# Kernel optimization log

Hardware: AMD Instinct MI355X
Metric: run time of the kernel (lower is better)

Reference implementation:

```python
import jax, jax.numpy as jnp
import numpy as np

B, T, C = 4, 4096, 1024
NEG_INF = -1e38


def setup_inputs() -> dict:
    key = jax.random.key(0)
    ks = jax.random.split(key, 5)
    scale = 0.02  # realistic init scale for CxC projections
    x = jax.random.normal(ks[0], (B, T, C), dtype=jnp.float32)
    key_w = jax.random.normal(ks[1], (C, C), dtype=jnp.float32) * scale
    value_w = jax.random.normal(ks[2], (C, C), dtype=jnp.float32) * scale
    receptance_w = jax.random.normal(ks[3], (C, C), dtype=jnp.float32) * scale
    output_w = jax.random.normal(ks[4], (C, C), dtype=jnp.float32) * scale
    # deterministic param init matching the module's __init__
    time_decay = -5.0 + 8.0 * (jnp.arange(C, dtype=jnp.float32) / (C - 1)) ** 0.7
    time_first = jnp.full((C,), -3.0, dtype=jnp.float32)
    # initial WKV state as in forward() when state is None
    aa0 = jnp.zeros((B, C), dtype=jnp.float32)
    bb0 = jnp.zeros((B, C), dtype=jnp.float32)
    pp0 = jnp.full((B, C), NEG_INF, dtype=jnp.float32)
    return dict(x=x, key_w=key_w, value_w=value_w, receptance_w=receptance_w,
                output_w=output_w, time_decay=time_decay, time_first=time_first,
                aa0=aa0, bb0=bb0, pp0=pp0)


def reference(x, key_w, value_w, receptance_w, output_w,
              time_decay, time_first, aa0, bb0, pp0):
    # projections (torch Linear: y = x @ W.T)
    k = jnp.einsum('btc,dc->btd', x, key_w)        # [B,T,C]
    v = jnp.einsum('btc,dc->btd', x, value_w)      # [B,T,C]
    r = jax.nn.sigmoid(jnp.einsum('btc,dc->btd', x, receptance_w))
    w = jnp.exp(time_decay)  # [C]
    u = time_first           # [C]

    def step(carry, kv):
        aa, bb, pp = carry           # each [B,C]
        kt, vt = kv                  # each [B,C]
        # output at this step (numerically stabilized exp weighting)
        ww = u + kt
        p = jnp.maximum(pp, ww)
        e1 = jnp.exp(pp - p)
        e2 = jnp.exp(ww - p)
        wkv = (e1 * aa + e2 * vt) / (e1 * bb + e2)
        # state update
        ww2 = pp - w
        p2 = jnp.maximum(ww2, kt)
        e1b = jnp.exp(ww2 - p2)
        e2b = jnp.exp(kt - p2)
        return (e1b * aa + e2b * vt, e1b * bb + e2b, p2), wkv

    k_t = jnp.swapaxes(k, 0, 1)  # [T,B,C]
    v_t = jnp.swapaxes(v, 0, 1)
    (aa, bb, pp), wkv = jax.lax.scan(step, (aa0, bb0, pp0), (k_t, v_t))
    wkv = jnp.swapaxes(wkv, 0, 1)  # [B,T,C]

    out = jnp.einsum('btc,dc->btd', r * wkv, output_w)
    return out, aa, bb, pp
```

## Files before the change

### kernel.cpp

```cpp
#include <hip/hip_runtime.h>
#include <stdint.h>

#define BDIM 4
#define TDIM 4096
#define CDIM 1024
#define MDIM (BDIM * TDIM)
#define SSEG 64
#define LSEG 64
#define NCH  (BDIM * CDIM)

#define GK   1024
#define GK2  2048
#define NTK  16

typedef __attribute__((ext_vector_type(8))) short bf16x8;
typedef __attribute__((ext_vector_type(4))) float f32x4;

__device__ __forceinline__ unsigned short f2bf(float f) {
    unsigned u = __builtin_bit_cast(unsigned, f);
    u = u + 0x7fffu + ((u >> 16) & 1u);
    return (unsigned short)(u >> 16);
}
__device__ __forceinline__ float bf2f(unsigned short h) {
    unsigned u = ((unsigned)h) << 16;
    return __builtin_bit_cast(float, u);
}

typedef __attribute__((address_space(1))) const unsigned int g_u32;
typedef __attribute__((address_space(3))) unsigned int l_u32;
__device__ __forceinline__ void gload_lds16(const void* g, void* l) {
    __builtin_amdgcn_global_load_lds((g_u32*)g, (l_u32*)l, 16, 0, 0);
}

__global__ void castall(const float* __restrict__ x,
                        const float* __restrict__ kw, const float* __restrict__ vw,
                        const float* __restrict__ rw, const float* __restrict__ ow,
                        unsigned short* __restrict__ xb,
                        unsigned short* __restrict__ wf, unsigned short* __restrict__ owb) {
    int i = blockIdx.x * 256 + threadIdx.x;
    const float* s;
    unsigned short* d;
    int j;
    if (i < 4194304) {
        s = x; d = xb; j = i;
    } else {
        int k = i - 4194304;
        int m = k >> 18; j = k & 262143;
        s = (m == 0) ? kw : (m == 1) ? vw : (m == 2) ? rw : ow;
        d = (m < 3) ? (wf + (size_t)m * 1048576) : owb;
    }
    float4 f = ((const float4*)s)[j];
    ushort4 o;
    o.x = f2bf(f.x); o.y = f2bf(f.y); o.z = f2bf(f.z); o.w = f2bf(f.w);
    ((ushort4*)d)[j] = o;
}

template <int MODE, int NT>
__global__ __launch_bounds__(512, 2) void gemm256(
    const unsigned short* __restrict__ A,
    const unsigned short* __restrict__ Bw,
    unsigned short* __restrict__ oK, unsigned short* __restrict__ oV,
    unsigned short* __restrict__ oR, float* __restrict__ oF)
{
    extern __shared__ char sh[];
    char* shA = sh;
    char* shB = sh + 65536;

    const int tid  = threadIdx.x;
    const int wave = tid >> 6;
    const int lane = tid & 63;
    const int wm   = wave >> 2;
    const int wn   = wave & 3;
    const int lrow = lane & 15;
    const int koct = lane >> 4;

    const int kb0 = (koct * 16) ^ ((lrow & 7) << 4);
    const int kb1 = kb0 ^ 64;

    const int sr0  = tid >> 3;
    const int sc0  = ((tid & 7) * 16) ^ ((sr0 & 7) << 4);
    const int sr1  = (512 + tid) >> 3;
    const int sc1  = ((tid & 7) * 16) ^ ((sr1 & 7) << 4);
    const int sd0  = tid * 16;
    const int sd1  = 8192 + tid * 16;

    const int bid = blockIdx.x;
    const int xcd = bid & 7;
    const int idx = bid >> 3;
    const int mt  = xcd * 8 + idx / NT;
    const int nt  = idx % NT;
    const size_t row0 = (size_t)mt * 256;
    const size_t col0 = (size_t)nt * 256;

    const char* gA = (const char*)A  + row0 * GK2;
    const char* gB = (const char*)Bw + col0 * GK2;

    auto stage = [&](int tt, int part) {
        if (tt >= NTK) return;
        int slot = tt & 1;
        int isA  = (part < 2) ? 1 : 0;
        int half = part & 1;
        const char* gbase = (isA ? gA : gB) + (size_t)half * 128 * GK2 + tt * 128;
        char* lbase = (isA ? shA : shB) + (slot * 2 + half) * 16384;
        gload_lds16(gbase + (size_t)sr0 * GK2 + sc0, lbase + sd0);
        gload_lds16(gbase + (size_t)sr1 * GK2 + sc1, lbase + sd1);
    };

    stage(0, 0); stage(0, 1); stage(0, 2); stage(0, 3);
    stage(1, 0); stage(1, 1);
    asm volatile("s_waitcnt vmcnt(4)" ::: "memory");
    __builtin_amdgcn_s_barrier();

    f32x4 acc[8][4] = {};
    bf16x8 af[8][2], bf_[4][2];

    {
        const char* ab0 = shA + wm * 16384 + lrow * 128;
#pragma unroll
        for (int mi = 0; mi < 4; ++mi) {
            af[mi][0] = *(const bf16x8*)(ab0 + mi * 2048 + kb0);
            af[mi][1] = *(const bf16x8*)(ab0 + mi * 2048 + kb1);
        }
    }

    for (int t = 0; t < NTK; ++t) {
        const int slot  = t & 1;
        const char* ab  = shA + (slot * 2 + wm) * 16384 + lrow * 128;
        const char* bb  = shB + (slot * 2 + (wn >> 1)) * 16384 + ((wn & 1) * 64 + lrow) * 128;
        const char* abN = shA + (((t + 1) & 1) * 2 + wm) * 16384 + lrow * 128;

#pragma unroll
        for (int ni = 0; ni < 4; ++ni) {
            bf_[ni][0] = *(const bf16x8*)(bb + ni * 2048 + kb0);
            bf_[ni][1] = *(const bf16x8*)(bb + ni * 2048 + kb1);
        }
#pragma unroll
        for (int mi = 4; mi < 8; ++mi) {
            af[mi][0] = *(const bf16x8*)(ab + mi * 2048 + kb0);
            af[mi][1] = *(const bf16x8*)(ab + mi * 2048 + kb1);
        }
        stage(t + 1, 2);
        stage(t + 1, 3);
        __builtin_amdgcn_s_barrier();
        __builtin_amdgcn_s_setprio(1);
#pragma unroll
        for (int a = 0; a < 4; ++a)
#pragma unroll
            for (int b = 0; b < 4; ++b)
#pragma unroll
                for (int ks = 0; ks < 2; ++ks)
                    acc[a][b] = __builtin_amdgcn_mfma_f32_16x16x32_bf16(af[a][ks], bf_[b][ks], acc[a][b], 0, 0, 0);
        __builtin_amdgcn_s_setprio(0);
        if (t <= 14)      asm volatile("s_waitcnt vmcnt(4)" ::: "memory");
        __builtin_amdgcn_s_barrier();

        if (t + 1 < NTK) {
#pragma unroll
            for (int mi = 0; mi < 4; ++mi) {
                af[mi][0] = *(const bf16x8*)(abN + mi * 2048 + kb0);
                af[mi][1] = *(const bf16x8*)(abN + mi * 2048 + kb1);
            }
        }
        stage(t + 2, 0);
        stage(t + 2, 1);
        __builtin_amdgcn_s_barrier();
        __builtin_amdgcn_s_setprio(1);
#pragma unroll
        for (int a = 0; a < 4; ++a)
#pragma unroll
            for (int b = 0; b < 4; ++b)
#pragma unroll
                for (int ks = 0; ks < 2; ++ks)
                    acc[4 + a][b] = __builtin_amdgcn_mfma_f32_16x16x32_bf16(af[4 + a][ks], bf_[b][ks], acc[4 + a][b], 0, 0, 0);
        __builtin_amdgcn_s_setprio(0);
        if (t <= 13)      asm volatile("s_waitcnt vmcnt(4)" ::: "memory");
        else if (t == 14) asm volatile("s_waitcnt vmcnt(0)" ::: "memory");
        __builtin_amdgcn_s_barrier();
    }

    const int crow = (lane >> 4) * 4;
    const int ccol = lane & 15;
    if (MODE == 1) {
#pragma unroll
        for (int mi = 0; mi < 8; ++mi)
#pragma unroll
            for (int ni = 0; ni < 4; ++ni) {
                size_t gr = row0 + wm * 128 + mi * 16 + crow;
                size_t gc = col0 + wn * 64 + ni * 16 + ccol;
#pragma unroll
                for (int j = 0; j < 4; ++j)
                    oF[(gr + j) * 1024 + gc] = acc[mi][ni][j];
            }
    } else {
        const int region = nt >> 2;
        unsigned short* dst = (region == 0) ? oK : ((region == 1) ? oV : oR);
        const size_t cb0 = (size_t)(nt & 3) * 256;
#pragma unroll
        for (int mi = 0; mi < 8; ++mi)
#pragma unroll
            for (int ni = 0; ni < 4; ++ni) {
                size_t gr = row0 + wm * 128 + mi * 16 + crow;
                size_t gc = cb0 + wn * 64 + ni * 16 + ccol;
#pragma unroll
                for (int j = 0; j < 4; ++j) {
                    float val = acc[mi][ni][j];
                    if (region == 2) val = 1.0f / (1.0f + __expf(-val));
                    dst[(gr + j) * 1024 + gc] = f2bf(val);
                }
            }
    }
}

__global__ __launch_bounds__(256) void wkv_phase1(
    const unsigned short* __restrict__ kf, const unsigned short* __restrict__ vf,
    const float* __restrict__ td,
    float* __restrict__ segA, float* __restrict__ segB, float* __restrict__ segP)
{
    const int tid  = blockIdx.x * 256 + threadIdx.x;
    const int lane = tid & 63;
    const int wg   = tid >> 6;
    const int cg   = wg & 63;
    const int s    = wg >> 6;
    const int q    = cg * 64 + lane;
    const int b    = q >> 10;
    const int c    = q & (CDIM - 1);

    const float w = __expf(td[c]);

    float aa = 0.0f, bb = 0.0f, pp = -1e38f;
    size_t idx = (size_t)b * TDIM * CDIM + (size_t)(s * LSEG) * CDIM + c;
#pragma unroll 4
    for (int i = 0; i < LSEG; ++i, idx += CDIM) {
        float kt = bf2f(kf[idx]);
        float vt = bf2f(vf[idx]);
        float ww2 = pp - w;
        float p2  = fmaxf(ww2, kt);
        float e1  = __expf(ww2 - p2);
        float e2  = __expf(kt - p2);
        aa = e1 * aa + e2 * vt;
        bb = e1 * bb + e2;
        pp = p2;
    }
    segA[s * NCH + q] = aa;
    segB[s * NCH + q] = bb;
    segP[s * NCH + q] = pp;
}

__global__ __launch_bounds__(256) void wkv_phase2(
    const float* __restrict__ segA, const float* __restrict__ segB, const float* __restrict__ segP,
    const float* __restrict__ td,
    const float* __restrict__ aa0, const float* __restrict__ bb0, const float* __restrict__ pp0,
    float* __restrict__ preA, float* __restrict__ preB, float* __restrict__ preP,
    float* __restrict__ stout)
{
    const int tid = blockIdx.x * 256 + threadIdx.x;
    const int c = tid & (CDIM - 1);
    const float w  = __expf(td[c]);
    const float Lw = (float)LSEG * w;

    float aa = aa0[tid], bb = bb0[tid], pp = pp0[tid];
    for (int s = 0; s < SSEG; ++s) {
        preA[s * NCH + tid] = aa;
        preB[s * NCH + tid] = bb;
        preP[s * NCH + tid] = pp;
        float al = segA[s * NCH + tid];
        float bl = segB[s * NCH + tid];
        float pl = segP[s * NCH + tid];
        float ppd = pp - Lw;
        float p  = fmaxf(ppd, pl);
        float e1 = __expf(ppd - p);
        float e2 = __expf(pl - p);
        aa = e1 * aa + e2 * al;
        bb = e1 * bb + e2 * bl;
        pp = p;
    }
    stout[tid]           = aa;
    stout[NCH + tid]     = bb;
    stout[2 * NCH + tid] = pp;
}

__global__ __launch_bounds__(256) void wkv_phase3(
    const unsigned short* __restrict__ kf, const unsigned short* __restrict__ vf,
    const unsigned short* __restrict__ rb,
    const float* __restrict__ td, const float* __restrict__ tf,
    const float* __restrict__ preA, const float* __restrict__ preB, const float* __restrict__ preP,
    unsigned short* __restrict__ rwkvb)
{
    const int tid  = blockIdx.x * 256 + threadIdx.x;
    const int lane = tid & 63;
    const int wg   = tid >> 6;
    const int cg   = wg & 63;
    const int s    = wg >> 6;
    const int q    = cg * 64 + lane;
    const int b    = q >> 10;
    const int c    = q & (CDIM - 1);

    const float w = __expf(td[c]);
    const float u = tf[c];

    float aa = preA[s * NCH + q];
    float bb = preB[s * NCH + q];
    float pp = preP[s * NCH + q];

    size_t idx = (size_t)b * TDIM * CDIM + (size_t)(s * LSEG) * CDIM + c;
#pragma unroll 4
    for (int i = 0; i < LSEG; ++i, idx += CDIM) {
        float kt = bf2f(kf[idx]);
        float vt = bf2f(vf[idx]);
        float rt = bf2f(rb[idx]);
        float ww = u + kt;
        float p  = fmaxf(pp, ww);
        float e1 = __expf(pp - p);
        float e2 = __expf(ww - p);
        float wkv = (e1 * aa + e2 * vt) / (e1 * bb + e2);
        rwkvb[idx] = f2bf(rt * wkv);
        float ww2 = pp - w;
        float p2  = fmaxf(ww2, kt);
        float e1b = __expf(ww2 - p2);
        float e2b = __expf(kt - p2);
        aa = e1b * aa + e2b * vt;
        bb = e1b * bb + e2b;
        pp = p2;
    }
}

extern "C" void kernel_launch(void* const* d_in, const int* in_sizes, int n_in,
                              void* d_out, int out_size, void* d_ws, size_t ws_size,
                              hipStream_t stream) {
    const float* x   = (const float*)d_in[0];
    const float* kw  = (const float*)d_in[1];
    const float* vw  = (const float*)d_in[2];
    const float* rw  = (const float*)d_in[3];
    const float* ow  = (const float*)d_in[4];
    const float* td  = (const float*)d_in[5];
    const float* tf  = (const float*)d_in[6];
    const float* aa0 = (const float*)d_in[7];
    const float* bb0 = (const float*)d_in[8];
    const float* pp0 = (const float*)d_in[9];
    float* out = (float*)d_out;

    char* ws = (char*)d_ws;
    unsigned short* wf    = (unsigned short*)(ws);
    unsigned short* owb   = (unsigned short*)(ws + 6291456);
    unsigned short* xb    = (unsigned short*)(ws + 8388608);
    unsigned short* kfb   = (unsigned short*)(ws + 41943040);
    unsigned short* vfb   = (unsigned short*)(ws + 75497472);
    unsigned short* rbb   = (unsigned short*)(ws + 109051904);
    unsigned short* rwkvb = (unsigned short*)(ws + 142606336);
    float* segA = (float*)(ws + 176160768);
    float* segB = (float*)(ws + 177209344);
    float* segP = (float*)(ws + 178257920);
    float* preA = (float*)(ws + 179306496);
    float* preB = (float*)(ws + 180355072);
    float* preP = (float*)(ws + 181403648);

    hipFuncSetAttribute((const void*)(gemm256<0, 12>), hipFuncAttributeMaxDynamicSharedMemorySize, 131072);
    hipFuncSetAttribute((const void*)(gemm256<1, 4>),  hipFuncAttributeMaxDynamicSharedMemorySize, 131072);

    castall<<<20480, 256, 0, stream>>>(x, kw, vw, rw, ow, xb, wf, owb);

    gemm256<0, 12><<<768, 512, 131072, stream>>>(xb, wf, kfb, vfb, rbb, nullptr);

    wkv_phase1<<<NCH * SSEG / 256, 256, 0, stream>>>(kfb, vfb, td, segA, segB, segP);
    wkv_phase2<<<NCH / 256, 256, 0, stream>>>(segA, segB, segP, td, aa0, bb0, pp0,
                                              preA, preB, preP, out + (size_t)MDIM * CDIM);
    wkv_phase3<<<NCH * SSEG / 256, 256, 0, stream>>>(kfb, vfb, rbb, td, tf,
                                                     preA, preB, preP, rwkvb);

    gemm256<1, 4><<<256, 512, 131072, stream>>>(rwkvb, owb, nullptr, nullptr, nullptr, out);
}
```

Before: 219.5 us.

## Restructure GEMM mainloop to 32-wide K tiles with four-stage LDS pipeline

The GEMM main loop now steps through K in 32-element tiles (64 bytes) instead of 64-element tiles, keeping four LDS slots in flight with three tiles prefetched. The swizzled LDS layout is reworked so each fragment is one 16-byte read, and B fragments are double-buffered in registers across iterations. The goal is deeper prefetch to hide global-load latency at the same LDS footprint. In exchange there are twice as many barriers and waitcnt points per unit of K work, and each global load row is shorter.

```diff
diff --git a/kernel.cpp b/kernel.cpp
--- a/kernel.cpp
+++ b/kernel.cpp
@@ -11,7 +11,7 @@
 
 #define GK   1024
 #define GK2  2048
-#define NTK  16
+#define NT32 32
 
 typedef __attribute__((ext_vector_type(8))) short bf16x8;
 typedef __attribute__((ext_vector_type(4))) float f32x4;
@@ -55,6 +55,49 @@
     ((ushort4*)d)[j] = o;
 }
 
+
+#define MFMA16(ACCROW, AREG, BREG)                                          \
+    _Pragma("unroll") for (int a_ = 0; a_ < 4; ++a_)                        \
+    _Pragma("unroll") for (int b_ = 0; b_ < 4; ++b_)                        \
+        acc[ACCROW + a_][b_] = __builtin_amdgcn_mfma_f32_16x16x32_bf16(     \
+            AREG[a_], BREG[b_], acc[ACCROW + a_][b_], 0, 0, 0);
+
+#define KT32(T, BU, BN)                                                     \
+  {                                                                         \
+    const int slot  = (T) & 3;                                              \
+    const int slotN = ((T) + 1) & 3;                                        \
+                          \
+    {                                                                       \
+        const char* ab = shA + slot * 16384 + wm * 8192 + aoffc;            \
+        _Pragma("unroll") for (int m_ = 0; m_ < 4; ++m_)                    \
+            a47[m_] = *(const bf16x8*)(ab + (4 + m_) * 1024);               \
+    }                                                                       \
+    stage((T) + 3, 0);                                                      \
+    __builtin_amdgcn_s_barrier();                                           \
+    __builtin_amdgcn_s_setprio(1);                                          \
+    MFMA16(0, a03, BU)                                                      \
+    __builtin_amdgcn_s_setprio(0);                                          \
+    if ((T) <= 28)      asm volatile("s_waitcnt vmcnt(6)" ::: "memory");    \
+    else if ((T) == 29) asm volatile("s_waitcnt vmcnt(4)" ::: "memory");    \
+    else if ((T) == 30) asm volatile("s_waitcnt vmcnt(0)" ::: "memory");    \
+    __builtin_amdgcn_s_barrier();                                           \
+                \
+    if ((T) + 1 < NT32) {                                                   \
+        const char* abN = shA + slotN * 16384 + wm * 8192 + aoffc;          \
+        const char* bbN = shB + slotN * 16384 + wn * 4096 + aoffc;          \
+        _Pragma("unroll") for (int m_ = 0; m_ < 4; ++m_)                    \
+            a03[m_] = *(const bf16x8*)(abN + m_ * 1024);                    \
+        _Pragma("unroll") for (int n_ = 0; n_ < 4; ++n_)                    \
+            BN[n_] = *(const bf16x8*)(bbN + n_ * 1024);                     \
+    }                                                                       \
+    stage((T) + 3, 1);                                                      \
+    __builtin_amdgcn_s_barrier();                                           \
+    __builtin_amdgcn_s_setprio(1);                                          \
+    MFMA16(4, a47, BU)                                                      \
+    __builtin_amdgcn_s_setprio(0);                                          \
+    __builtin_amdgcn_s_barrier();                                           \
+  }
+
 template <int MODE, int NT>
 __global__ __launch_bounds__(512, 2) void gemm256(
     const unsigned short* __restrict__ A,
@@ -74,13 +117,12 @@
     const int lrow = lane & 15;
     const int koct = lane >> 4;
 
-    const int kb0 = (koct * 16) ^ ((lrow & 7) << 4);
-    const int kb1 = kb0 ^ 64;
-
-    const int sr0  = tid >> 3;
-    const int sc0  = ((tid & 7) * 16) ^ ((sr0 & 7) << 4);
-    const int sr1  = (512 + tid) >> 3;
-    const int sc1  = ((tid & 7) * 16) ^ ((sr1 & 7) << 4);
+    const int aoffc = (lrow >> 1) * 128 +
+                      ((((lrow & 1) * 64) + koct * 16) ^ (((lrow >> 1) & 7) << 4));
+
+    const int inl  = ((tid & 7) * 16) ^ (((tid >> 3) & 7) << 4);
+    const int sg0r = 2 * (tid >> 3) + (inl >> 6);
+    const int sgc  = inl & 63;
     const int sd0  = tid * 16;
     const int sd1  = 8192 + tid * 16;
 
@@ -95,87 +137,36 @@
     const char* gA = (const char*)A  + row0 * GK2;
     const char* gB = (const char*)Bw + col0 * GK2;
 
-    auto stage = [&](int tt, int part) {
-        if (tt >= NTK) return;
-        int slot = tt & 1;
-        int isA  = (part < 2) ? 1 : 0;
-        int half = part & 1;
-        const char* gbase = (isA ? gA : gB) + (size_t)half * 128 * GK2 + tt * 128;
-        char* lbase = (isA ? shA : shB) + (slot * 2 + half) * 16384;
-        gload_lds16(gbase + (size_t)sr0 * GK2 + sc0, lbase + sd0);
-        gload_lds16(gbase + (size_t)sr1 * GK2 + sc1, lbase + sd1);
+    auto stage = [&](int tt, int isB) {
+        if (tt >= NT32) return;
+        int slot = tt & 3;
+        const char* gbase = (isB ? gB : gA) + tt * 64;
+        char* lbase = (isB ? shB : shA) + slot * 16384;
+        gload_lds16(gbase + (size_t)sg0r * GK2 + sgc, lbase + sd0);
+        gload_lds16(gbase + (size_t)(sg0r + 128) * GK2 + sgc, lbase + sd1);
     };
 
-    stage(0, 0); stage(0, 1); stage(0, 2); stage(0, 3);
+    stage(0, 0); stage(0, 1);
     stage(1, 0); stage(1, 1);
-    asm volatile("s_waitcnt vmcnt(4)" ::: "memory");
+    stage(2, 0); stage(2, 1);
+    asm volatile("s_waitcnt vmcnt(8)" ::: "memory");
     __builtin_amdgcn_s_barrier();
 
     f32x4 acc[8][4] = {};
-    bf16x8 af[8][2], bf_[4][2];
+    bf16x8 a03[4], a47[4], bA[4], bB[4];
 
     {
-        const char* ab0 = shA + wm * 16384 + lrow * 128;
-#pragma unroll
-        for (int mi = 0; mi < 4; ++mi) {
-            af[mi][0] = *(const bf16x8*)(ab0 + mi * 2048 + kb0);
-            af[mi][1] = *(const bf16x8*)(ab0 + mi * 2048 + kb1);
-        }
-    }
-
-    for (int t = 0; t < NTK; ++t) {
-        const int slot  = t & 1;
-        const char* ab  = shA + (slot * 2 + wm) * 16384 + lrow * 128;
-        const char* bb  = shB + (slot * 2 + (wn >> 1)) * 16384 + ((wn & 1) * 64 + lrow) * 128;
-        const char* abN = shA + (((t + 1) & 1) * 2 + wm) * 16384 + lrow * 128;
-
-#pragma unroll
-        for (int ni = 0; ni < 4; ++ni) {
-            bf_[ni][0] = *(const bf16x8*)(bb + ni * 2048 + kb0);
-            bf_[ni][1] = *(const bf16x8*)(bb + ni * 2048 + kb1);
-        }
-#pragma unroll
-        for (int mi = 4; mi < 8; ++mi) {
-            af[mi][0] = *(const bf16x8*)(ab + mi * 2048 + kb0);
-            af[mi][1] = *(const bf16x8*)(ab + mi * 2048 + kb1);
-        }
-        stage(t + 1, 2);
-        stage(t + 1, 3);
-        __builtin_amdgcn_s_barrier();
-        __builtin_amdgcn_s_setprio(1);
-#pragma unroll
-        for (int a = 0; a < 4; ++a)
-#pragma unroll
-            for (int b = 0; b < 4; ++b)
-#pragma unroll
-                for (int ks = 0; ks < 2; ++ks)
-                    acc[a][b] = __builtin_amdgcn_mfma_f32_16x16x32_bf16(af[a][ks], bf_[b][ks], acc[a][b], 0, 0, 0);
-        __builtin_amdgcn_s_setprio(0);
-        if (t <= 14)      asm volatile("s_waitcnt vmcnt(4)" ::: "memory");
-        __builtin_amdgcn_s_barrier();
-
-        if (t + 1 < NTK) {
-#pragma unroll
-            for (int mi = 0; mi < 4; ++mi) {
-                af[mi][0] = *(const bf16x8*)(abN + mi * 2048 + kb0);
-                af[mi][1] = *(const bf16x8*)(abN + mi * 2048 + kb1);
-            }
-        }
-        stage(t + 2, 0);
-        stage(t + 2, 1);
-        __builtin_amdgcn_s_barrier();
-        __builtin_amdgcn_s_setprio(1);
-#pragma unroll
-        for (int a = 0; a < 4; ++a)
-#pragma unroll
-            for (int b = 0; b < 4; ++b)
-#pragma unroll
-                for (int ks = 0; ks < 2; ++ks)
-                    acc[4 + a][b] = __builtin_amdgcn_mfma_f32_16x16x32_bf16(af[4 + a][ks], bf_[b][ks], acc[4 + a][b], 0, 0, 0);
-        __builtin_amdgcn_s_setprio(0);
-        if (t <= 13)      asm volatile("s_waitcnt vmcnt(4)" ::: "memory");
-        else if (t == 14) asm volatile("s_waitcnt vmcnt(0)" ::: "memory");
-        __builtin_amdgcn_s_barrier();
+        const char* ab0 = shA + wm * 8192 + aoffc;
+        const char* bb0 = shB + wn * 4096 + aoffc;
+#pragma unroll
+        for (int m = 0; m < 4; ++m) a03[m] = *(const bf16x8*)(ab0 + m * 1024);
+#pragma unroll
+        for (int n = 0; n < 4; ++n) bA[n] = *(const bf16x8*)(bb0 + n * 1024);
+    }
+
+    for (int tt = 0; tt < NT32; tt += 2) {
+        KT32(tt,     bA, bB)
+        KT32(tt + 1, bB, bA)
     }
 
     const int crow = (lane >> 4) * 4;
```

Result: slower. 226.3 us (+3.1%).
